# Kernel tuning notes

Hardware: AMD Instinct MI355X
Metric: run time of the kernel (lower is better)

The kernel has to match this reference:

```python
import jax, jax.numpy as jnp
import numpy as np

N, D, K = 4096, 1024, 32
MARGIN = 0.3
OP_TYPE = "weighty"


def setup_inputs() -> dict:
    key = jax.random.key(0)
    k1, k2, k3, k4, k5 = jax.random.split(key, 5)
    return {
        "inputs": jax.random.normal(k1, (N, D), jnp.float32),
        "prediction": jax.random.normal(k2, (N, K), jnp.float32),
        "targets": jax.random.randint(k3, (N,), 0, K),
        "true_targets": jax.random.randint(k4, (N,), 0, K),
        "prob": jax.random.uniform(k5, (N,), jnp.float32),
        "threshold": jnp.float32(0.5),
    }


def _weighty(d1, d2, pair_type, op_type):
    # vectorized translation of weighty_new
    if op_type == "mean":
        return (d1 + d2) / 2.0
    if op_type == "max":
        return jnp.maximum(d1, d2)
    if op_type == "min":
        return jnp.minimum(d1, d2)
    if op_type == "max-min":
        return jnp.maximum(d1, d2) if pair_type == 1 else jnp.minimum(d1, d2)
    # op_type == 'weighty'
    if pair_type == 1:
        e1, e2 = jnp.exp(d1), jnp.exp(d2)
        return (e1 * d1 + e2 * d2) / (e1 + e2)
    e1, e2 = jnp.exp(-d1), jnp.exp(-d2)
    return (e1 * d1 + e2 * d2) / (e1 + e2 + 1e-6)


def reference(inputs, prediction, targets, true_targets, prob, threshold):
    n = inputs.shape[0]
    rows = jnp.arange(n)
    # pairwise euclidean dist (GEMM-based, matches addmm_ formulation)
    sq = jnp.sum(inputs * inputs, axis=1)
    dist = sq[:, None] + sq[None, :] - 2.0 * (inputs @ inputs.T)
    dist = jnp.sqrt(jnp.clip(dist, 1e-12, None))  # [n, n]

    same = targets[:, None] == targets[None, :]
    conf = prob >= threshold

    # negatives sorted ascending by dist; positives sorted descending by dist
    neg_order = jnp.argsort(jnp.where(~same, dist, jnp.inf), axis=1)   # [n,n]
    pos_order = jnp.argsort(jnp.where(same, -dist, jnp.inf), axis=1)   # [n,n]
    hp = pos_order[:, 0]   # hardest positive (max dist)
    hn = neg_order[:, 0]   # hardest negative (min dist)
    d_ap = dist[rows, hp]
    d_an = dist[rows, hn]

    cp = prob[hp] >= threshold
    cn = prob[hn] >= threshold
    fn = jnp.argmax(prediction, axis=1)[hn] == targets  # hard neg is a false negative

    # neg re-selection: ranks 1..10 first with prob>=t, else rank 11 (loop_cnt cap 10)
    neg_cand = neg_order[:, 1:12]                       # [n,11]
    ok_n = prob[neg_cand] >= threshold
    sel_n = jnp.where(ok_n[:, :10].any(axis=1), jnp.argmax(ok_n[:, :10], axis=1), 10)
    d_nn = dist[rows, neg_cand[rows, sel_n]]

    # pos re-selection: descending ranks 1..5 first with prob>=t, else rank 6 (loop_cnt cap 5)
    pos_cand = pos_order[:, 1:7]                        # [n,6]
    ok_p = prob[pos_cand] >= threshold
    sel_p = jnp.where(ok_p[:, :5].any(axis=1), jnp.argmax(ok_p[:, :5], axis=1), 5)
    d_np = dist[rows, pos_cand[rows, sel_p]]

    w1 = _weighty(d_ap, d_an, 1, OP_TYPE)
    w0 = _weighty(d_ap, d_an, 0, OP_TYPE)

    case_b = cp & (~cn) & fn                 # confident pos, unconfident FN neg
    case_cd = (~cp) & (cn | (~fn))           # unconfident pos branches that re-select pos
    inv = (~cp) & (~cn) & fn                 # inverse loss branch

    ap = jnp.where(case_b, w1, jnp.where(case_cd, d_np, d_ap))
    an = jnp.where(case_b, d_nn, jnp.where(case_cd, w0, d_an))

    per = jnp.where(inv,
                    jax.nn.relu(an - ap + MARGIN),
                    jax.nn.relu(ap - an + MARGIN))
    conff = conf.astype(per.dtype)
    cnt = jnp.sum(conf.astype(jnp.int32))
    loss = jnp.where(cnt > 0, jnp.sum(per * conff) / jnp.maximum(cnt, 1).astype(per.dtype), 0.0)
    correct = jnp.sum(((an >= ap) & conf).astype(jnp.int32))
    return loss, correct, cnt
```

## Files before the change

### kernel.cpp

```cpp
#include <hip/hip_runtime.h>
#include <hip/hip_bf16.h>
#include <stdint.h>

typedef _Float16 half8 __attribute__((ext_vector_type(8)));
typedef _Float16 half4 __attribute__((ext_vector_type(4)));
typedef float f32x4 __attribute__((ext_vector_type(4)));
typedef unsigned short ushort8v __attribute__((ext_vector_type(8)));
typedef unsigned short ushort4v __attribute__((ext_vector_type(4)));
typedef unsigned long long u64;

#define N_ROWS 4096
#define DIM 1024
#define KCLS 32
#define MARGIN_F 0.3f

typedef const __attribute__((address_space(1))) void GASV;
typedef __attribute__((address_space(3))) void LASV;

__device__ __forceinline__ void gload_lds16(const void* g, void* l) {
    __builtin_amdgcn_global_load_lds((GASV*)g, (LASV*)l, 16, 0, 0);
}

__global__ __launch_bounds__(256) void prep_kernel(
    const float* __restrict__ inputs, const float* __restrict__ prediction,
    _Float16* __restrict__ xh, float* __restrict__ sq, int* __restrict__ pred_cls)
{
    int wid = threadIdx.x >> 6, lane = threadIdx.x & 63;
    int r = blockIdx.x * 4 + wid;
    const float* row = inputs + (size_t)r * DIM;
    _Float16* hrow = xh + (size_t)r * DIM;
    float s = 0.f;
#pragma unroll
    for (int c = 0; c < 4; ++c) {
        int idx = lane * 4 + c * 256;
        float4 v = *(const float4*)(row + idx);
        s += v.x * v.x + v.y * v.y + v.z * v.z + v.w * v.w;
        half4 h;
        h.x = (_Float16)v.x; h.y = (_Float16)v.y;
        h.z = (_Float16)v.z; h.w = (_Float16)v.w;
        *(half4*)(hrow + idx) = h;
    }
#pragma unroll
    for (int off = 32; off; off >>= 1) s += __shfl_xor(s, off);

    u64 key = 0ull;
    if (lane < KCLS) {
        unsigned b = __float_as_uint(prediction[(size_t)r * KCLS + lane]);
        unsigned u = (b & 0x80000000u) ? ~b : (b | 0x80000000u);
        key = ((u64)u << 32) | (unsigned)(KCLS - 1 - lane);
    }
#pragma unroll
    for (int off = 32; off; off >>= 1) {
        u64 o = __shfl_xor(key, off);
        if (o > key) key = o;
    }
    if (lane == 0) {
        sq[r] = s;
        pred_cls[r] = KCLS - 1 - (int)(key & 0xFFFFFFFFu);
    }
}

__global__ __launch_bounds__(512) void gemm_kernel(
    const _Float16* __restrict__ X, const float* __restrict__ sq,
    const int* __restrict__ targets,
    unsigned short* __restrict__ out, int mode, int rb0)
{
    __shared__ __align__(16) _Float16 As[2 * 128 * 64];
    __shared__ __align__(16) _Float16 Bs[2 * 128 * 64];
    int tid = threadIdx.x;

    int bx, by;
    bool mirror = false;
    if (mode == 0) {
        int u = ((int)blockIdx.x & 7) * 66 + ((int)blockIdx.x >> 3);
        int t_ = (int)((sqrtf(8.f * u + 1.f) - 1.f) * 0.5f);
        while ((t_ + 1) * (t_ + 2) / 2 <= u) ++t_;
        while (t_ * (t_ + 1) / 2 > u) --t_;
        by = t_;
        bx = u - t_ * (t_ + 1) / 2;
        mirror = (bx != by);
    } else {
        int nwg = gridDim.x;
        int q = nwg >> 3;
        int swz = ((int)blockIdx.x & 7) * q + ((int)blockIdx.x >> 3);
        int nbx = nwg / 32;
        bx = swz % nbx;
        by = swz / nbx;
    }

    int rs = tid >> 3;
    int ss = tid & 7;
    int srcslot = ss ^ (rs & 7);
    const _Float16* gA = X + (size_t)(rb0 + bx * 128 + rs) * DIM + srcslot * 8;
    const _Float16* gB = X + (size_t)(by * 128 + rs) * DIM + srcslot * 8;
    _Float16* lA = As + tid * 8;
    _Float16* lB = Bs + tid * 8;

    int wid = tid >> 6, lane = tid & 63;
    int wr = (wid >> 2) * 64, wc = (wid & 3) * 32;
    int fr = lane & 15, q4 = lane >> 4;

    f32x4 acc[4][2];
#pragma unroll
    for (int m = 0; m < 4; ++m)
#pragma unroll
        for (int n = 0; n < 2; ++n) acc[m][n] = (f32x4){0.f, 0.f, 0.f, 0.f};

    auto STAGE = [&](int buf, int t) {
        int k0 = t * 64;
#pragma unroll
        for (int p = 0; p < 2; ++p) {
            gload_lds16(gA + k0 + (size_t)(p * 64) * DIM, lA + buf * 8192 + p * 4096);
            gload_lds16(gB + k0 + (size_t)(p * 64) * DIM, lB + buf * 8192 + p * 4096);
        }
    };
    auto COMPUTE = [&](int buf) {
        const _Float16* Ac = As + buf * 8192;
        const _Float16* Bc = Bs + buf * 8192;
#pragma unroll
        for (int ks = 0; ks < 2; ++ks) {
            half8 a[4], b[2];
#pragma unroll
            for (int m = 0; m < 4; ++m) {
                int row = wr + m * 16 + fr;
                int s = (ks * 4 + q4) ^ (row & 7);
                a[m] = *(const half8*)(Ac + row * 64 + s * 8);
            }
#pragma unroll
            for (int n = 0; n < 2; ++n) {
                int brow = wc + n * 16 + fr;
                int s = (ks * 4 + q4) ^ (brow & 7);
                b[n] = *(const half8*)(Bc + brow * 64 + s * 8);
            }
            __builtin_amdgcn_s_setprio(1);
#pragma unroll
            for (int m = 0; m < 4; ++m)
#pragma unroll
                for (int n = 0; n < 2; ++n)
                    acc[m][n] = __builtin_amdgcn_mfma_f32_16x16x32_f16(a[m], b[n], acc[m][n], 0, 0, 0);
            __builtin_amdgcn_s_setprio(0);
        }
    };

    STAGE(0, 0);
    STAGE(1, 1);

    int cur = 0;
    for (int t = 0; t < 15; ++t) {
        asm volatile("s_waitcnt vmcnt(4)" ::: "memory");
        __builtin_amdgcn_s_barrier();
        __builtin_amdgcn_sched_barrier(0);
        COMPUTE(cur);
        __builtin_amdgcn_sched_barrier(0);
        __builtin_amdgcn_s_barrier();
        __builtin_amdgcn_sched_barrier(0);
        if (t + 2 < 16) STAGE(cur, t + 2);
        cur ^= 1;
    }
    asm volatile("s_waitcnt vmcnt(0)" ::: "memory");
    __builtin_amdgcn_s_barrier();
    __builtin_amdgcn_sched_barrier(0);
    COMPUTE(cur);

    int rbase = rb0 + bx * 128 + wr + q4 * 4;
    float sqr_[4][4];
    int trr[4][4];
#pragma unroll
    for (int m = 0; m < 4; ++m)
#pragma unroll
        for (int q = 0; q < 4; ++q) {
            sqr_[m][q] = sq[rbase + m * 16 + q];
            trr[m][q] = targets[rbase + m * 16 + q];
        }

#pragma unroll
    for (int n = 0; n < 2; ++n) {
        int col = by * 128 + wc + n * 16 + fr;
        float sqc = sq[col];
        int tc = targets[col];
#pragma unroll
        for (int m = 0; m < 4; ++m) {
            int row0 = rbase + m * 16;
            ushort4v hv;
#pragma unroll
            for (int q = 0; q < 4; ++q) {
                float d2v = fmaxf(sqr_[m][q] + sqc - 2.f * acc[m][n][q], 1e-12f);
                _Float16 h = (_Float16)d2v;
                unsigned short hb = __builtin_bit_cast(unsigned short, h);
                hb = (unsigned short)(hb | ((trr[m][q] == tc) ? 0x8000u : 0u));
                hv[q] = hb;
                out[(size_t)(row0 + q) * N_ROWS + col] = hb;
            }
            if (mirror)
                *(ushort4v*)&out[(size_t)col * N_ROWS + row0] = hv;
        }
    }
}

__global__ __launch_bounds__(256) void select_kernel(
    const unsigned short* __restrict__ dot,
    const int* __restrict__ targets, const float* __restrict__ prob,
    const int* __restrict__ pred_cls, const float* __restrict__ thr_p,
    int rb0, float* __restrict__ per_term, int* __restrict__ corr_flag)
{
    __shared__ unsigned Tn[4], Tp[4];
    __shared__ unsigned negCand[64];
    __shared__ unsigned posCand[64];
    __shared__ unsigned cnts[2];
    __shared__ unsigned sN[12], sP[7];
    __shared__ unsigned red[4];
    __shared__ unsigned bcast;

    int t = threadIdx.x, lane = t & 63, w = t >> 6;
    int rloc = blockIdx.x, r = rb0 + rloc;
    const unsigned short* drow = dot + (size_t)rloc * N_ROWS;

    if (t < 64) { negCand[t] = 0xFFFFFFFFu; posCand[t] = 0u; }
    if (t < 2) cnts[t] = 0u;

    unsigned short hb[16];
    unsigned mneg = 0xFFFFFFFFu, mpos = 0u;
    {
        ushort8v v0 = *(const ushort8v*)(drow + t * 8);
        ushort8v v1 = *(const ushort8v*)(drow + 2048 + t * 8);
#pragma unroll
        for (int j = 0; j < 8; ++j) {
            unsigned b = v0[j]; hb[j] = (unsigned short)b;
            mneg = b < mneg ? b : mneg;
            mpos = b > mpos ? b : mpos;
        }
#pragma unroll
        for (int j = 0; j < 8; ++j) {
            unsigned b = v1[j]; hb[8 + j] = (unsigned short)b;
            mneg = b < mneg ? b : mneg;
            mpos = b > mpos ? b : mpos;
        }
    }

    unsigned T3 = 0xFFFFFFFFu, m = mneg;
#pragma unroll
    for (int rd = 0; rd < 3; ++rd) {
        unsigned b = m;
#pragma unroll
        for (int off = 32; off; off >>= 1) {
            unsigned o = __shfl_xor(b, off);
            b = o < b ? o : b;
        }
        T3 = b;
        if (m == b) m = 0xFFFFFFFFu;
    }
    unsigned P2 = 0u, mp = mpos;
#pragma unroll
    for (int rd = 0; rd < 2; ++rd) {
        unsigned b = mp;
#pragma unroll
        for (int off = 32; off; off >>= 1) {
            unsigned o = __shfl_xor(b, off);
            b = o > b ? o : b;
        }
        P2 = b;
        if (mp == b) mp = 0u;
    }
    if (lane == 0) { Tn[w] = T3; Tp[w] = P2; }
    __syncthreads();

    unsigned TnB = Tn[0];
    TnB = Tn[1] > TnB ? Tn[1] : TnB;
    TnB = Tn[2] > TnB ? Tn[2] : TnB;
    TnB = Tn[3] > TnB ? Tn[3] : TnB;
    unsigned TpB = Tp[0];
    TpB = Tp[1] < TpB ? Tp[1] : TpB;
    TpB = Tp[2] < TpB ? Tp[2] : TpB;
    TpB = Tp[3] < TpB ? Tp[3] : TpB;

#pragma unroll
    for (int j = 0; j < 16; ++j) {
        int col = (j < 8) ? (t * 8 + j) : (2048 + t * 8 + (j - 8));
        unsigned b = hb[j];
        if (!(b & 0x8000u) && b <= TnB) {
            unsigned s = atomicAdd(&cnts[0], 1u);
            if (s < 64u) negCand[s] = (b << 16) | (unsigned)col;
        }
        if ((b & 0x8000u) && b >= TpB) {
            unsigned s = atomicAdd(&cnts[1], 1u);
            if (s < 64u) posCand[s] = (b << 16) | (unsigned)(N_ROWS - 1 - col);
        }
    }
    __syncthreads();

    bool fb = (cnts[0] > 64u) || (cnts[1] > 64u);

    if (!fb) {
        if (w == 0) {
            unsigned v = negCand[lane];
#pragma unroll
            for (int k = 2; k <= 64; k <<= 1) {
#pragma unroll
                for (int j = 32; j; j >>= 1) {
                    if (j >= k) continue;
                    unsigned o = __shfl_xor(v, j);
                    bool up = (lane & k) == 0;
                    bool small = (lane & j) == 0;
                    bool keepmin = (small == up);
                    unsigned lo = v < o ? v : o, hi = v < o ? o : v;
                    v = keepmin ? lo : hi;
                }
            }
            if (lane < 12) sN[lane] = v;
        } else if (w == 1) {
            unsigned v = ~posCand[lane];
#pragma unroll
            for (int k = 2; k <= 64; k <<= 1) {
#pragma unroll
                for (int j = 32; j; j >>= 1) {
                    if (j >= k) continue;
                    unsigned o = __shfl_xor(v, j);
                    bool up = (lane & k) == 0;
                    bool small = (lane & j) == 0;
                    bool keepmin = (small == up);
                    unsigned lo = v < o ? v : o, hi = v < o ? o : v;
                    v = keepmin ? lo : hi;
                }
            }
            if (lane < 7) sP[lane] = ~v;
        }
    } else {
        unsigned remN = 0, remP = 0;
        for (int rd = 0; rd < 12; ++rd) {
            unsigned best = 0xFFFFFFFFu;
#pragma unroll
            for (int j = 0; j < 16; ++j) {
                int col = (j < 8) ? (t * 8 + j) : (2048 + t * 8 + (j - 8));
                unsigned b = hb[j];
                bool valid = !(b & 0x8000u) && !((remN >> j) & 1u);
                unsigned nk = valid ? ((b << 16) | (unsigned)col) : 0xFFFFFFFFu;
                best = nk < best ? nk : best;
            }
#pragma unroll
            for (int off = 32; off; off >>= 1) {
                unsigned o = __shfl_xor(best, off);
                best = o < best ? o : best;
            }
            if (lane == 0) red[w] = best;
            __syncthreads();
            if (t == 0) {
                unsigned b0 = red[0];
                b0 = red[1] < b0 ? red[1] : b0;
                b0 = red[2] < b0 ? red[2] : b0;
                b0 = red[3] < b0 ? red[3] : b0;
                sN[rd] = b0; bcast = b0;
            }
            __syncthreads();
            unsigned b0 = bcast;
#pragma unroll
            for (int j = 0; j < 16; ++j) {
                int col = (j < 8) ? (t * 8 + j) : (2048 + t * 8 + (j - 8));
                if ((((unsigned)hb[j] << 16) | (unsigned)col) == b0) remN |= 1u << j;
            }
            __syncthreads();
        }
        for (int rd = 0; rd < 7; ++rd) {
            unsigned best = 0u;
#pragma unroll
            for (int j = 0; j < 16; ++j) {
                int col = (j < 8) ? (t * 8 + j) : (2048 + t * 8 + (j - 8));
                unsigned b = hb[j];
                bool valid = (b & 0x8000u) && !((remP >> j) & 1u);
                unsigned pk = valid ? ((b << 16) | (unsigned)(N_ROWS - 1 - col)) : 0u;
                best = pk > best ? pk : best;
            }
#pragma unroll
            for (int off = 32; off; off >>= 1) {
                unsigned o = __shfl_xor(best, off);
                best = o > best ? o : best;
            }
            if (lane == 0) red[w] = best;
            __syncthreads();
            if (t == 0) {
                unsigned b0 = red[0];
                b0 = red[1] > b0 ? red[1] : b0;
                b0 = red[2] > b0 ? red[2] : b0;
                b0 = red[3] > b0 ? red[3] : b0;
                sP[rd] = b0; bcast = b0;
            }
            __syncthreads();
            unsigned b0 = bcast;
#pragma unroll
            for (int j = 0; j < 16; ++j) {
                int col = (j < 8) ? (t * 8 + j) : (2048 + t * 8 + (j - 8));
                if ((((unsigned)hb[j] << 16) | (unsigned)(N_ROWS - 1 - col)) == b0) remP |= 1u << j;
            }
            __syncthreads();
        }
    }
    __syncthreads();

    if (w == 0) {
        float thr = *thr_p;
        int tr = targets[r];
        unsigned kN = (lane < 12) ? sN[lane] : 0xFFFFFFFFu;
        unsigned kP = (lane >= 32 && lane < 39) ? sP[lane - 32] : 0u;
        int idxN = (int)(kN & 0xFFFFu) & (N_ROWS - 1);
        int idxP = (N_ROWS - 1 - (int)(kP & 0xFFFFu)) & (N_ROWS - 1);
        bool confN = (lane < 12) && kN != 0xFFFFFFFFu && (prob[idxN] >= thr);
        bool confP = (lane >= 32 && lane < 39) && kP != 0u && (prob[idxP] >= thr);
        u64 balN = __ballot(confN);
        u64 balP = __ballot(confP);

        u64 mN_ = balN & 0x7FEull;
        int selN = mN_ ? (__ffsll(mN_) - 1) : 11;
        unsigned dnn_b = __shfl(kN >> 16, selN);
        u64 mP_ = balP & (0x3Eull << 32);
        int selP = mP_ ? (__ffsll(mP_) - 1) : 38;
        unsigned dnp_b = __shfl(kP >> 16, selP);
        unsigned dap_b = __shfl(kP >> 16, 32);

        if (lane == 0) {
            auto h2f = [](unsigned b16) -> float {
                unsigned short us = (unsigned short)(b16 & 0x7FFFu);
                _Float16 h = __builtin_bit_cast(_Float16, us);
                return (float)h;
            };
            float d_ap = sqrtf(h2f(dap_b));
            float d_an = sqrtf(h2f(kN >> 16));
            int hn = idxN;
            bool cp = (balP >> 32) & 1ull;
            bool cn = balN & 1ull;
            bool fn = (pred_cls[hn] == tr);
            float d_nn = sqrtf(h2f(dnn_b));
            float d_np = sqrtf(h2f(dnp_b));

            float e1p = __expf(d_ap), e2p = __expf(d_an);
            float w1 = (e1p * d_ap + e2p * d_an) / (e1p + e2p);
            float e1n = __expf(-d_ap), e2n = __expf(-d_an);
            float w0 = (e1n * d_ap + e2n * d_an) / (e1n + e2n + 1e-6f);
            bool case_b = cp && !cn && fn;
            bool case_cd = !cp && (cn || !fn);
            bool inv = !cp && !cn && fn;
            float ap = case_b ? w1 : (case_cd ? d_np : d_ap);
            float an = case_b ? d_nn : (case_cd ? w0 : d_an);
            float per = inv ? fmaxf(an - ap + MARGIN_F, 0.f)
                            : fmaxf(ap - an + MARGIN_F, 0.f);
            per_term[r] = per;
            corr_flag[r] = (an >= ap) ? 1 : 0;
        }
    }
}

__global__ __launch_bounds__(256) void finalize_kernel(
    const float* __restrict__ per_term, const int* __restrict__ corr_flag,
    const float* __restrict__ prob, const float* __restrict__ thr_p,
    float* __restrict__ out)
{
    __shared__ float sred[4]; __shared__ int cred[4]; __shared__ int nred[4];
    float thr = *thr_p;
    int t = threadIdx.x, lane = t & 63, wid = t >> 6;
    float s = 0.f; int c = 0, n = 0;
    for (int i = t; i < N_ROWS; i += 256) {
        if (prob[i] >= thr) {
            s += per_term[i];
            c += corr_flag[i];
            n += 1;
        }
    }
#pragma unroll
    for (int off = 32; off; off >>= 1) {
        s += __shfl_xor(s, off);
        c += __shfl_xor(c, off);
        n += __shfl_xor(n, off);
    }
    if (lane == 0) { sred[wid] = s; cred[wid] = c; nred[wid] = n; }
    __syncthreads();
    if (t == 0) {
        float ss = sred[0] + sred[1] + sred[2] + sred[3];
        int cc = cred[0] + cred[1] + cred[2] + cred[3];
        int nn = nred[0] + nred[1] + nred[2] + nred[3];
        float loss = (nn > 0) ? ss / (float)nn : 0.f;
        out[0] = loss;
        out[1] = (float)cc;
        out[2] = (float)nn;
    }
}

extern "C" void kernel_launch(void* const* d_in, const int* in_sizes, int n_in,
                              void* d_out, int out_size, void* d_ws, size_t ws_size,
                              hipStream_t stream)
{
    const float* inputs     = (const float*)d_in[0];
    const float* prediction = (const float*)d_in[1];
    const int*   targets    = (const int*)d_in[2];
    const float* prob       = (const float*)d_in[4];
    const float* thr        = (const float*)d_in[5];
    float* out = (float*)d_out;

    char* ws = (char*)d_ws;
    size_t off = 0;
    auto alloc = [&](size_t bytes) -> char* {
        char* p = ws + off;
        off = (off + bytes + 255) & ~(size_t)255;
        return p;
    };
    _Float16* xh     = (_Float16*)alloc((size_t)N_ROWS * DIM * sizeof(_Float16));
    float* sq        = (float*)alloc((size_t)N_ROWS * 4);
    int*   pred_cls  = (int*)alloc((size_t)N_ROWS * 4);
    float* per_term  = (float*)alloc((size_t)N_ROWS * 4);
    int*   corr_flag = (int*)alloc((size_t)N_ROWS * 4);

    size_t avail = (ws_size > off) ? (ws_size - off) : 0;
    size_t rowbytes = (size_t)N_ROWS * 2;
    int RB = 128;
    while (RB * 2 <= N_ROWS && (size_t)(RB * 2) * rowbytes <= avail) RB *= 2;
    unsigned short* dotbuf = (unsigned short*)alloc((size_t)RB * rowbytes);

    hipLaunchKernelGGL(prep_kernel, dim3(N_ROWS / 4), dim3(256), 0, stream,
                       inputs, prediction, xh, sq, pred_cls);
    if (RB == N_ROWS) {
        hipLaunchKernelGGL(gemm_kernel, dim3(528), dim3(512), 0, stream,
                           xh, sq, targets, dotbuf, 0, 0);
        hipLaunchKernelGGL(select_kernel, dim3(N_ROWS), dim3(256), 0, stream,
                           dotbuf, targets, prob, pred_cls, thr, 0,
                           per_term, corr_flag);
    } else {
        for (int rb0 = 0; rb0 < N_ROWS; rb0 += RB) {
            hipLaunchKernelGGL(gemm_kernel, dim3((RB / 128) * 32), dim3(512), 0, stream,
                               xh, sq, targets, dotbuf, 1, rb0);
            hipLaunchKernelGGL(select_kernel, dim3(RB), dim3(256), 0, stream,
                               dotbuf, targets, prob, pred_cls, thr, rb0,
                               per_term, corr_flag);
        }
    }
    hipLaunchKernelGGL(finalize_kernel, dim3(1), dim3(256), 0, stream,
                       per_term, corr_flag, prob, thr, out);
}
```

Measured before the change: 70.91 us.

## Switch GEMM pipeline to four-stage K=32 buffering with deeper prefetch

Restructures the fp16 GEMM main loop from a double-buffered K=64 tile to a four-buffer ring of K=32 tiles. More loads are kept in flight (waiting on vmcnt(6)), and the tail is peeled into four explicit compute steps. The intent is to hide global-to-LDS latency better at the same LDS footprint. The cost is twice as many barrier pairs per K, less MFMA work between syncs, and a narrower 4-slot XOR swizzle that may increase LDS bank conflicts.

```diff
diff --git a/kernel.cpp b/kernel.cpp
--- a/kernel.cpp
+++ b/kernel.cpp
@@ -65,8 +65,8 @@
     const int* __restrict__ targets,
     unsigned short* __restrict__ out, int mode, int rb0)
 {
-    __shared__ __align__(16) _Float16 As[2 * 128 * 64];
-    __shared__ __align__(16) _Float16 Bs[2 * 128 * 64];
+    __shared__ __align__(16) _Float16 As[4 * 128 * 32];
+    __shared__ __align__(16) _Float16 Bs[4 * 128 * 32];
     int tid = threadIdx.x;
 
     int bx, by;
@@ -88,9 +88,9 @@
         by = swz / nbx;
     }
 
-    int rs = tid >> 3;
-    int ss = tid & 7;
-    int srcslot = ss ^ (rs & 7);
+    int rs = tid >> 2;
+    int ss = tid & 3;
+    int srcslot = ss ^ (rs & 3);
     const _Float16* gA = X + (size_t)(rb0 + bx * 128 + rs) * DIM + srcslot * 8;
     const _Float16* gB = X + (size_t)(by * 128 + rs) * DIM + srcslot * 8;
     _Float16* lA = As + tid * 8;
@@ -107,60 +107,66 @@
         for (int n = 0; n < 2; ++n) acc[m][n] = (f32x4){0.f, 0.f, 0.f, 0.f};
 
     auto STAGE = [&](int buf, int t) {
-        int k0 = t * 64;
-#pragma unroll
-        for (int p = 0; p < 2; ++p) {
-            gload_lds16(gA + k0 + (size_t)(p * 64) * DIM, lA + buf * 8192 + p * 4096);
-            gload_lds16(gB + k0 + (size_t)(p * 64) * DIM, lB + buf * 8192 + p * 4096);
-        }
+        int k0 = t * 32;
+        gload_lds16(gA + k0, lA + buf * 4096);
+        gload_lds16(gB + k0, lB + buf * 4096);
     };
     auto COMPUTE = [&](int buf) {
-        const _Float16* Ac = As + buf * 8192;
-        const _Float16* Bc = Bs + buf * 8192;
-#pragma unroll
-        for (int ks = 0; ks < 2; ++ks) {
-            half8 a[4], b[2];
-#pragma unroll
-            for (int m = 0; m < 4; ++m) {
-                int row = wr + m * 16 + fr;
-                int s = (ks * 4 + q4) ^ (row & 7);
-                a[m] = *(const half8*)(Ac + row * 64 + s * 8);
-            }
-#pragma unroll
-            for (int n = 0; n < 2; ++n) {
-                int brow = wc + n * 16 + fr;
-                int s = (ks * 4 + q4) ^ (brow & 7);
-                b[n] = *(const half8*)(Bc + brow * 64 + s * 8);
-            }
-            __builtin_amdgcn_s_setprio(1);
-#pragma unroll
-            for (int m = 0; m < 4; ++m)
-#pragma unroll
-                for (int n = 0; n < 2; ++n)
-                    acc[m][n] = __builtin_amdgcn_mfma_f32_16x16x32_f16(a[m], b[n], acc[m][n], 0, 0, 0);
-            __builtin_amdgcn_s_setprio(0);
-        }
+        const _Float16* Ac = As + buf * 4096;
+        const _Float16* Bc = Bs + buf * 4096;
+        half8 a[4], b[2];
+#pragma unroll
+        for (int m = 0; m < 4; ++m) {
+            int row = wr + m * 16 + fr;
+            int s = q4 ^ (row & 3);
+            a[m] = *(const half8*)(Ac + row * 32 + s * 8);
+        }
+#pragma unroll
+        for (int n = 0; n < 2; ++n) {
+            int brow = wc + n * 16 + fr;
+            int s = q4 ^ (brow & 3);
+            b[n] = *(const half8*)(Bc + brow * 32 + s * 8);
+        }
+        __builtin_amdgcn_s_setprio(1);
+#pragma unroll
+        for (int m = 0; m < 4; ++m)
+#pragma unroll
+            for (int n = 0; n < 2; ++n)
+                acc[m][n] = __builtin_amdgcn_mfma_f32_16x16x32_f16(a[m], b[n], acc[m][n], 0, 0, 0);
+        __builtin_amdgcn_s_setprio(0);
     };
 
-    STAGE(0, 0);
-    STAGE(1, 1);
-
-    int cur = 0;
-    for (int t = 0; t < 15; ++t) {
-        asm volatile("s_waitcnt vmcnt(4)" ::: "memory");
+    STAGE(0, 0); STAGE(1, 1); STAGE(2, 2); STAGE(3, 3);
+
+    for (int t = 0; t < 28; ++t) {
+        asm volatile("s_waitcnt vmcnt(6)" ::: "memory");
         __builtin_amdgcn_s_barrier();
         __builtin_amdgcn_sched_barrier(0);
-        COMPUTE(cur);
+        COMPUTE(t & 3);
         __builtin_amdgcn_sched_barrier(0);
         __builtin_amdgcn_s_barrier();
         __builtin_amdgcn_sched_barrier(0);
-        if (t + 2 < 16) STAGE(cur, t + 2);
-        cur ^= 1;
-    }
+        STAGE(t & 3, t + 4);
+    }
+    asm volatile("s_waitcnt vmcnt(6)" ::: "memory");
+    __builtin_amdgcn_s_barrier();
+    __builtin_amdgcn_sched_barrier(0);
+    COMPUTE(0);
+    __builtin_amdgcn_s_barrier();
+    asm volatile("s_waitcnt vmcnt(4)" ::: "memory");
+    __builtin_amdgcn_s_barrier();
+    __builtin_amdgcn_sched_barrier(0);
+    COMPUTE(1);
+    __builtin_amdgcn_s_barrier();
+    asm volatile("s_waitcnt vmcnt(2)" ::: "memory");
+    __builtin_amdgcn_s_barrier();
+    __builtin_amdgcn_sched_barrier(0);
+    COMPUTE(2);
+    __builtin_amdgcn_s_barrier();
     asm volatile("s_waitcnt vmcnt(0)" ::: "memory");
     __builtin_amdgcn_s_barrier();
     __builtin_amdgcn_sched_barrier(0);
-    COMPUTE(cur);
+    COMPUTE(3);
 
     int rbase = rb0 + bx * 128 + wr + q4 * 4;
     float sqr_[4][4];
```

New measurement: 77.28 us. +9.0%, slower.
